# Kernel tuning notes

Measured on AMD Instinct MI355X. Metric: run time of the kernel, lower is better.

Reference implementation:

```python
import jax, jax.numpy as jnp
import numpy as np
import math

B, QL, KL, D, H, FF = 2, 2048, 2048, 512, 8, 2048
DH = D // H

def layernorm(x, g, b, eps=1e-5):
    m = jnp.mean(x, axis=-1, keepdims=True)
    v = jnp.mean((x - m) ** 2, axis=-1, keepdims=True)
    return (x - m) * jax.lax.rsqrt(v + eps) * g + b

def mha(x, mask, wq, bq, wk, bk, wv, bv, wo, bo, kv=None):
    # faithful port of MultiHeadAttention.forward (eval mode, dropout off)
    bs, qlen, dim = x.shape
    src = x if kv is None else kv
    def split(t):
        return t.reshape(bs, -1, H, DH).transpose(0, 2, 1, 3)  # [b,h,l,dh]
    q = split(x @ wq + bq) * (1.0 / math.sqrt(DH))
    k = split(src @ wk + bk)
    v = split(src @ wv + bv)
    scores = jnp.einsum('bhqd,bhkd->bhqk', q, k)
    m = mask[:, None, :, :] if mask.ndim == 3 else mask[:, None, None, :]
    scores = jnp.where(m == 0, -jnp.inf, scores)
    w = jax.nn.softmax(scores.astype(jnp.float32), axis=-1).astype(scores.dtype)
    ctx = jnp.einsum('bhqk,bhkd->bhqd', w, v)
    ctx = ctx.transpose(0, 2, 1, 3).reshape(bs, qlen, dim)
    return ctx @ wo + bo

def decoder_layer(tgt, memory, pos, tkpm, causal_mask, mem_mask,
                  sa, ca, l1w, l1b, l2w, l2b, n1g, n1b, n2g, n2b, n3g, n3b):
    tgt = tgt + pos
    t2 = layernorm(tgt, n1g, n1b)
    t2 = t2 * tkpm[:, :, None]
    t2 = mha(t2, causal_mask, *sa)
    tgt = tgt + t2
    t2 = layernorm(tgt, n2g, n2b)
    t2 = mha(t2, mem_mask, *ca, kv=memory)
    tgt = tgt + t2
    t2 = layernorm(tgt, n3g, n3b)
    t2 = jax.nn.relu(t2 @ l1w + l1b) @ l2w + l2b
    tgt = tgt + t2
    tgt = tgt * tkpm[:, :, None]
    return tgt

def setup_inputs() -> dict:
    key = jax.random.key(0)
    ks = jax.random.split(key, 32)
    it = iter(list(ks))
    def nrm(shape, s=0.02):
        return jax.random.normal(next(it), shape, jnp.float32) * s
    inp = {}
    inp['cfg'] = 0
    inp['tgt'] = jax.random.normal(next(it), (B, QL, D), jnp.float32)
    inp['memory'] = jax.random.normal(next(it), (B, KL, D), jnp.float32)
    inp['pos'] = jax.random.normal(next(it), (B, QL, D), jnp.float32)
    inp['causal_mask'] = jnp.broadcast_to(jnp.tril(jnp.ones((QL, QL), jnp.int32)), (B, QL, QL))
    inp['tgt_key_padding_mask'] = jnp.ones((B, QL), jnp.float32)
    mkpm = jax.random.randint(next(it), (B, KL), 0, 2).astype(jnp.int32)
    inp['memory_key_padding_mask'] = mkpm.at[:, 0].set(1)  # avoid fully-masked rows
    for p in ['sa', 'ca']:
        for w in ['q', 'k', 'v', 'o']:
            inp[f'{p}_{w}_w'] = nrm((D, D))
            inp[f'{p}_{w}_b'] = jnp.zeros((D,), jnp.float32)
    inp['lin1_w'] = nrm((D, FF)); inp['lin1_b'] = jnp.zeros((FF,), jnp.float32)
    inp['lin2_w'] = nrm((FF, D)); inp['lin2_b'] = jnp.zeros((D,), jnp.float32)
    for n in ['n1', 'n2', 'n3']:
        inp[f'{n}_g'] = jnp.ones((D,), jnp.float32)
        inp[f'{n}_b'] = jnp.zeros((D,), jnp.float32)
    return inp

def reference(cfg, tgt, memory, pos, causal_mask, tgt_key_padding_mask, memory_key_padding_mask,
              sa_q_w, sa_q_b, sa_k_w, sa_k_b, sa_v_w, sa_v_b, sa_o_w, sa_o_b,
              ca_q_w, ca_q_b, ca_k_w, ca_k_b, ca_v_w, ca_v_b, ca_o_w, ca_o_b,
              lin1_w, lin1_b, lin2_w, lin2_b,
              n1_g, n1_b, n2_g, n2_b, n3_g, n3_b):
    sa = (sa_q_w, sa_q_b, sa_k_w, sa_k_b, sa_v_w, sa_v_b, sa_o_w, sa_o_b)
    ca = (ca_q_w, ca_q_b, ca_k_w, ca_k_b, ca_v_w, ca_v_b, ca_o_w, ca_o_b)
    return decoder_layer(tgt, memory, pos, tgt_key_padding_mask, causal_mask, memory_key_padding_mask,
                         sa, ca, lin1_w, lin1_b, lin2_w, lin2_b, n1_g, n1_b, n2_g, n2_b, n3_g, n3_b)
```

## Files before the change

kernel.cpp:

```cpp
#include <hip/hip_runtime.h>
#include <hip/hip_bf16.h>
#include <stdint.h>

#define QL   2048
#define KLn  2048
#define DIM  512
#define NH   8
#define DH   64
#define NB   2
#define MROWS (NB*QL)
#define FFD  2048

typedef unsigned short u16;
typedef unsigned int u32;
typedef __attribute__((ext_vector_type(8))) short short8;
typedef __attribute__((ext_vector_type(4))) float f32x4;

__device__ __forceinline__ u16 f2b(float f){
  union { float f; u32 i; } v; v.f = f;
  u32 r = v.i + 0x7FFFu + ((v.i >> 16) & 1u);
  return (u16)(r >> 16);
}
__device__ __forceinline__ float b2f(u16 u){
  union { u32 i; float f; } v; v.i = ((u32)u) << 16; return v.f;
}
__device__ __forceinline__ u32 cvtpk(float a, float b){
  u32 r;
  asm("v_cvt_pk_bf16_f32 %0, %1, %2" : "=v"(r) : "v"(a), "v"(b));
  return r;
}

typedef __attribute__((address_space(3))) void as3void;
typedef __attribute__((address_space(1))) void as1void;
__device__ __forceinline__ void gload_lds16(const void* g, void* l){
  __builtin_amdgcn_global_load_lds((as1void*)g, (as3void*)l, 16, 0, 0);
}

#define BK 64
enum { EPI_BIAS=0, EPI_SCALEQ=1, EPI_RELU=2, EPI_RES=3, EPI_FIN=5, EPI_QKV=6, EPI_KV=7 };
#define QSCALE 0.1803368801111244f

template<int EPI>
__global__ __launch_bounds__(256, 4)
void gemm64(const u16* __restrict__ A, const u16* __restrict__ Bt,
            const float* __restrict__ bias,
            u16* __restrict__ Obf, float* __restrict__ Ores,
            const float* __restrict__ tk, float* __restrict__ fout,
            int K, int N)
{
  __shared__ __align__(16) u16 As[2][64*BK];
  __shared__ __align__(16) u16 Bs[2][64*BK];
  const int t  = threadIdx.x;
  const int l  = t & 63;
  const int lq = l & 15, lg = l >> 4;
  const int w  = t >> 6;
  const int wm = (w >> 1) * 32;
  const int wn = (w & 1) * 32;

  const int gx   = gridDim.x;
  const int nwg  = gx * gridDim.y;
  const int orig = blockIdx.x + gx * blockIdx.y;
  const int wgid = (orig & 7) * (nwg >> 3) + (orig >> 3);
  const int m0 = (wgid / gx) * 64;
  const int n0 = (wgid % gx) * 64;

  const int srow = t >> 3;
  const int scs  = t & 7;

  auto stageG = [&](u16* dA, u16* dB, int k0){
    _Pragma("unroll")
    for (int i = 0; i < 2; ++i){
      const int row = i*32 + srow;
      gload_lds16(A  + (size_t)(m0 + row)*K + k0 + ((scs ^ (row & 7)) << 3),
                  dA + row*BK + scs*8);
      gload_lds16(Bt + (size_t)(n0 + row)*K + k0 + ((scs ^ (row & 7)) << 3),
                  dB + row*BK + scs*8);
    }
  };

  int aoff[2][2], boff[2][2];
  _Pragma("unroll")
  for (int i = 0; i < 2; ++i)
    _Pragma("unroll")
    for (int kc = 0; kc < 2; ++kc){
      const int sw = (((kc*4 + lg) ^ (lq & 7)) << 3);
      aoff[i][kc] = ((wm + i*16 + lq)*BK + sw) * 2;
      boff[i][kc] = ((wn + i*16 + lq)*BK + sw) * 2;
    }

  f32x4 acc[2][2];
  _Pragma("unroll")
  for (int i=0;i<2;i++)
    _Pragma("unroll")
    for (int j=0;j<2;j++) acc[i][j] = (f32x4){0.f,0.f,0.f,0.f};

#define GBODY(BUF, KK)                                                        \
  {                                                                           \
    { const int ks = ((KK) + BK < K) ? (KK) + BK : 0;                         \
      stageG(As[(BUF)^1], Bs[(BUF)^1], ks); }                                 \
    asm volatile("s_waitcnt vmcnt(4)" ::: "memory");                          \
    __builtin_amdgcn_s_barrier();                                             \
    __builtin_amdgcn_sched_barrier(0);                                        \
    short8 af[2][2], bf[2][2];                                                \
    _Pragma("unroll")                                                         \
    for (int kc = 0; kc < 2; ++kc)                                            \
      _Pragma("unroll")                                                       \
      for (int i = 0; i < 2; ++i){                                            \
        af[i][kc] = *(const short8*)((const char*)As + (BUF)*8192 + aoff[i][kc]); \
        bf[i][kc] = *(const short8*)((const char*)Bs + (BUF)*8192 + boff[i][kc]); \
      }                                                                       \
    __builtin_amdgcn_s_barrier();                                             \
    __builtin_amdgcn_s_setprio(1);                                            \
    _Pragma("unroll")                                                         \
    for (int kc = 0; kc < 2; ++kc)                                            \
      _Pragma("unroll")                                                       \
      for (int i = 0; i < 2; ++i)                                             \
        _Pragma("unroll")                                                     \
        for (int j = 0; j < 2; ++j)                                           \
          acc[i][j] = __builtin_amdgcn_mfma_f32_16x16x32_bf16(af[i][kc], bf[j][kc], acc[i][j], 0,0,0); \
    __builtin_amdgcn_s_setprio(0);                                            \
  }

  stageG(As[0], Bs[0], 0);
  for (int k0 = 0; k0 < K; k0 += 2*BK){
    GBODY(0, k0)
    GBODY(1, k0 + BK)
  }
#undef GBODY

  _Pragma("unroll")
  for (int i=0;i<2;i++){
    _Pragma("unroll")
    for (int j=0;j<2;j++){
      _Pragma("unroll")
      for (int rr=0;rr<4;rr++){
        const int row = m0 + wm + i*16 + lg*4 + rr;
        const int col = n0 + wn + j*16 + lq;
        float v = acc[i][j][rr] + bias[col];
        if (EPI == EPI_SCALEQ) v *= QSCALE;
        if (EPI == EPI_RELU)   v = fmaxf(v, 0.f);
        if (EPI == EPI_RES)    Ores[(size_t)row*N + col] += v;
        else if (EPI == EPI_FIN){
          const size_t idx = (size_t)row*N + col;
          fout[idx] = (Ores[idx] + v) * tk[row];
        }
        else if (EPI == EPI_QKV){
          const int seg = col >> 9, c = col & 511;
          if (seg == 0)      Obf[(size_t)row*512 + c] = f2b(v * QSCALE);
          else if (seg == 1){
            const int bb = row >> 11, kv = row & 2047;
            const int hh = c >> 6,  dh = c & 63;
            Obf[(2u<<20) + ((((size_t)(bb*NH + hh) << 11) + kv) << 6) + (dh ^ ((kv & 7) << 3))] = f2b(v);
          }
          else               Obf[(4u<<20) + (size_t)row*512 + c] = f2b(v);
        }
        else if (EPI == EPI_KV){
          const int seg = col >> 9, c = col & 511;
          if (seg == 0){
            const int bb = row >> 11, kv = row & 2047;
            const int hh = c >> 6,  dh = c & 63;
            Obf[((((size_t)(bb*NH + hh) << 11) + kv) << 6) + (dh ^ ((kv & 7) << 3))] = f2b(v);
          }
          else               Obf[(2u<<20) + (size_t)row*512 + c] = f2b(v);
        }
        else                   Obf[(size_t)row*N + col] = f2b(v);
      }
    }
  }
}

template<bool CAUSAL>
__global__ __launch_bounds__(256, 2)
void attn8(const u16* __restrict__ Q, const u16* __restrict__ Kbh,
           const u16* __restrict__ Vth, const float* __restrict__ bias,
           u16* __restrict__ ctxp, float2* __restrict__ mlb)
{
  __shared__ __align__(16) u16 Kl[4][64*64];
  __shared__ __align__(16) u16 Vl[4][64*64];
  const int tid = threadIdx.x;
  const int l  = tid & 63;
  const int w  = tid >> 6;
  const int lq = l & 15, lg = l >> 4;
  const int h    = blockIdx.y;
  const int b    = blockIdx.z >> 1;
  const int half = blockIdx.z & 1;
  const int qtile = CAUSAL ? ((b & 1) ? (15 - (int)blockIdx.x) : (int)blockIdx.x)
                           : (int)blockIdx.x;
  const int rw = qtile*128 + w*32;

  const u16* kg = Kbh + ((size_t)(b*NH + h) << 17);
  const u16* vg = Vth + ((size_t)(b*NH + h) << 17);

  short8 aq[2][2];
  _Pragma("unroll")
  for (int g = 0; g < 2; ++g)
    _Pragma("unroll")
    for (int kc = 0; kc < 2; ++kc)
      aq[g][kc] = *(const short8*)(Q + (size_t)(b*QL + rw + g*16 + lq)*DIM + h*DH + kc*32 + lg*8);

  int koff[4][2];
  _Pragma("unroll")
  for (int j = 0; j < 4; ++j)
    _Pragma("unroll")
    for (int kc = 0; kc < 2; ++kc)
      koff[j][kc] = ((j*16 + lq)*64 + (((kc*4 + lg) ^ (lq & 7)) << 3)) * 2;

  f32x4 ctx[2][4];
  _Pragma("unroll")
  for (int g = 0; g < 2; ++g)
    _Pragma("unroll")
    for (int d = 0; d < 4; ++d) ctx[g][d] = (f32x4){0.f,0.f,0.f,0.f};
  f32x4 ls0 = (f32x4){0.f,0.f,0.f,0.f};
  f32x4 ls1 = (f32x4){0.f,0.f,0.f,0.f};
  float m0v = -1e30f, m1v = -1e30f;

  const int ntiles = CAUSAL ? (2*qtile + 2) : (KLn >> 6);
  const int P = (ntiles > half) ? ((ntiles - half + 1) >> 1) : 0;

  auto stageA = [&](u16* dK, u16* dV, int tile){
    const u16* kgs = kg + ((size_t)tile << 12);
    const u16* vgs = vg + tile*64;
    gload_lds16(kgs + w*1024 + l*8,       dK + w*1024 + l*8);
    gload_lds16(kgs + w*1024 + 512 + l*8, dK + w*1024 + 512 + l*8);
    gload_lds16(vgs + (size_t)(w*16 +     (l>>3))*KLn + (l&7)*8, dV + w*1024 + l*8);
    gload_lds16(vgs + (size_t)(w*16 + 8 + (l>>3))*KLn + (l&7)*8, dV + w*1024 + 512 + l*8);
  };

#define ABODY(BUF, II)                                                        \
  {                                                                           \
    const int TT = half + 2*(II);                                             \
    f32x4 bv[4];                                                              \
    if (!CAUSAL){                                                             \
      _Pragma("unroll")                                                       \
      for (int sub = 0; sub < 4; ++sub)                                       \
        bv[sub] = *(const f32x4*)(bias + b*KLn + TT*64 + sub*16 + lg*4);      \
    }                                                                         \
    { const int i2 = (II) + 2;                                                \
      const int ts = (i2 < P) ? half + 2*i2 : half;                           \
      stageA(Kl[((BUF)+2)&3], Vl[((BUF)+2)&3], ts); }                         \
    if (CAUSAL) asm volatile("s_waitcnt vmcnt(8)" ::: "memory");              \
    else        asm volatile("s_waitcnt vmcnt(12)" ::: "memory");             \
    __builtin_amdgcn_s_barrier();                                             \
    __builtin_amdgcn_sched_barrier(0);                                        \
    f32x4 s[2][4];                                                            \
    _Pragma("unroll")                                                         \
    for (int g = 0; g < 2; ++g)                                               \
      _Pragma("unroll")                                                       \
      for (int sub = 0; sub < 4; ++sub) s[g][sub] = (f32x4){0.f,0.f,0.f,0.f}; \
    __builtin_amdgcn_s_setprio(1);                                            \
    _Pragma("unroll")                                                         \
    for (int sub = 0; sub < 4; ++sub)                                         \
      _Pragma("unroll")                                                       \
      for (int kc = 0; kc < 2; ++kc){                                         \
        short8 bk = *(const short8*)((const char*)Kl + (BUF)*8192 + koff[sub][kc]); \
        s[0][sub] = __builtin_amdgcn_mfma_f32_16x16x32_bf16(bk, aq[0][kc], s[0][sub], 0,0,0); \
        s[1][sub] = __builtin_amdgcn_mfma_f32_16x16x32_bf16(bk, aq[1][kc], s[1][sub], 0,0,0); \
      }                                                                       \
    __builtin_amdgcn_s_setprio(0);                                            \
    if (CAUSAL){                                                              \
      if (TT*64 + 63 > rw){                                                   \
        _Pragma("unroll")                                                     \
        for (int g = 0; g < 2; ++g)                                           \
          _Pragma("unroll")                                                   \
          for (int sub = 0; sub < 4; ++sub)                                   \
            _Pragma("unroll")                                                 \
            for (int rr = 0; rr < 4; ++rr)                                    \
              if (TT*64 + sub*16 + lg*4 + rr > rw + g*16 + lq) s[g][sub][rr] = -1e30f; \
      }                                                                       \
    } else {                                                                  \
      _Pragma("unroll")                                                       \
      for (int g = 0; g < 2; ++g)                                             \
        _Pragma("unroll")                                                     \
        for (int sub = 0; sub < 4; ++sub) s[g][sub] += bv[sub];               \
    }                                                                         \
    float px0 = s[0][0][0], px1 = s[1][0][0];                                 \
    _Pragma("unroll")                                                         \
    for (int sub = 0; sub < 4; ++sub)                                         \
      _Pragma("unroll")                                                       \
      for (int rr = 0; rr < 4; ++rr){                                         \
        px0 = fmaxf(px0, s[0][sub][rr]);                                      \
        px1 = fmaxf(px1, s[1][sub][rr]);                                      \
      }                                                                       \
    if (!__all(px0 <= m0v + 8.0f && px1 <= m1v + 8.0f)){                      \
      px0 = fmaxf(px0, __shfl_xor(px0, 16));                                  \
      px0 = fmaxf(px0, __shfl_xor(px0, 32));                                  \
      px1 = fmaxf(px1, __shfl_xor(px1, 16));                                  \
      px1 = fmaxf(px1, __shfl_xor(px1, 32));                                  \
      const float mn0 = fmaxf(m0v, px0), mn1 = fmaxf(m1v, px1);               \
      const float c0 = exp2f(m0v - mn0), c1 = exp2f(m1v - mn1);               \
      ls0 *= c0; ls1 *= c1;                                                   \
      _Pragma("unroll")                                                       \
      for (int rr = 0; rr < 4; ++rr){                                         \
        const float b0 = __shfl(c0, lg*4 + rr), b1 = __shfl(c1, lg*4 + rr);   \
        _Pragma("unroll")                                                     \
        for (int d = 0; d < 4; ++d){ ctx[0][d][rr] *= b0; ctx[1][d][rr] *= b1; } \
      }                                                                       \
      m0v = mn0; m1v = mn1;                                                   \
    }                                                                         \
    u32 pk0[4][2], pk1[4][2];                                                 \
    _Pragma("unroll")                                                         \
    for (int sub = 0; sub < 4; ++sub){                                        \
      float a0 = exp2f(s[0][sub][0] - m0v), a1 = exp2f(s[0][sub][1] - m0v);   \
      float a2 = exp2f(s[0][sub][2] - m0v), a3 = exp2f(s[0][sub][3] - m0v);   \
      ls0 += (f32x4){a0, a1, a2, a3};                                         \
      pk0[sub][0] = cvtpk(a0, a1); pk0[sub][1] = cvtpk(a2, a3);               \
      float e0 = exp2f(s[1][sub][0] - m1v), e1 = exp2f(s[1][sub][1] - m1v);   \
      float e2 = exp2f(s[1][sub][2] - m1v), e3 = exp2f(s[1][sub][3] - m1v);   \
      ls1 += (f32x4){e0, e1, e2, e3};                                         \
      pk1[sub][0] = cvtpk(e0, e1); pk1[sub][1] = cvtpk(e2, e3);               \
    }                                                                         \
    union { u32 u[4]; short8 s8; } pA0, pA1, pB0, pB1;                        \
    pA0.u[0] = pk0[0][0]; pA0.u[1] = pk0[0][1]; pA0.u[2] = pk0[1][0]; pA0.u[3] = pk0[1][1]; \
    pA1.u[0] = pk0[2][0]; pA1.u[1] = pk0[2][1]; pA1.u[2] = pk0[3][0]; pA1.u[3] = pk0[3][1]; \
    pB0.u[0] = pk1[0][0]; pB0.u[1] = pk1[0][1]; pB0.u[2] = pk1[1][0]; pB0.u[3] = pk1[1][1]; \
    pB1.u[0] = pk1[2][0]; pB1.u[1] = pk1[2][1]; pB1.u[2] = pk1[3][0]; pB1.u[3] = pk1[3][1]; \
    __builtin_amdgcn_s_setprio(1);                                            \
    _Pragma("unroll")                                                         \
    for (int d0 = 0; d0 < 4; ++d0){                                           \
      short8 v0 = *(const short8*)((const char*)Vl + (BUF)*8192 + koff[d0][0]); \
      short8 v1 = *(const short8*)((const char*)Vl + (BUF)*8192 + koff[d0][1]); \
      ctx[0][d0] = __builtin_amdgcn_mfma_f32_16x16x32_bf16(pA0.s8, v0, ctx[0][d0], 0,0,0); \
      ctx[0][d0] = __builtin_amdgcn_mfma_f32_16x16x32_bf16(pA1.s8, v1, ctx[0][d0], 0,0,0); \
      ctx[1][d0] = __builtin_amdgcn_mfma_f32_16x16x32_bf16(pB0.s8, v0, ctx[1][d0], 0,0,0); \
      ctx[1][d0] = __builtin_amdgcn_mfma_f32_16x16x32_bf16(pB1.s8, v1, ctx[1][d0], 0,0,0); \
    }                                                                         \
    __builtin_amdgcn_s_setprio(0);                                            \
    __builtin_amdgcn_s_barrier();                                             \
  }

  if (P > 0){
    stageA(Kl[0], Vl[0], half);
    { const int ts1 = (1 < P) ? half + 2 : half;
      stageA(Kl[1], Vl[1], ts1); }
    for (int i = 0; i < P; i += 4){
      ABODY(0, i)
      if (i + 1 < P) ABODY(1, i + 1)
      if (i + 2 < P) ABODY(2, i + 2)
      if (i + 3 < P) ABODY(3, i + 3)
    }
  }
#undef ABODY

  float h0 = (ls0[0] + ls0[1]) + (ls0[2] + ls0[3]);
  float h1 = (ls1[0] + ls1[1]) + (ls1[2] + ls1[3]);
  h0 += __shfl_xor(h0, 16); h0 += __shfl_xor(h0, 32);
  h1 += __shfl_xor(h1, 16); h1 += __shfl_xor(h1, 32);
  if (lg == 0){
    mlb[((size_t)((half*NB + b)*NH + h) << 11) + rw + lq]      = make_float2(m0v, h0);
    mlb[((size_t)((half*NB + b)*NH + h) << 11) + rw + 16 + lq] = make_float2(m1v, h1);
  }
  u16* cp = ctxp + (size_t)half*MROWS*DIM;
  _Pragma("unroll")
  for (int g = 0; g < 2; ++g)
    _Pragma("unroll")
    for (int d0 = 0; d0 < 4; ++d0)
      _Pragma("unroll")
      for (int rr = 0; rr < 4; ++rr)
        cp[(size_t)(b*QL + rw + g*16 + lg*4 + rr)*DIM + h*DH + d0*16 + lq] =
            f2b(ctx[g][d0][rr]);
}

__global__ __launch_bounds__(256)
void attn_merge(const u16* __restrict__ ctxp, const float2* __restrict__ mlb,
                u16* __restrict__ O)
{
  const int idx = blockIdx.x*256 + threadIdx.x;
  const int row = idx >> 7;
  const int col = (idx & 127) * 4;
  const int b = row >> 11, qr = row & 2047, h = col >> 6;
  const float2 a0 = mlb[((size_t)((      b)*NH + h) << 11) + qr];
  const float2 a1 = mlb[((size_t)((NB  + b)*NH + h) << 11) + qr];
  const float mg = fmaxf(a0.x, a1.x);
  const float w0 = exp2f(a0.x - mg), w1 = exp2f(a1.x - mg);
  const float rden = 1.f / (a0.y*w0 + a1.y*w1);
  union { uint2 v; u16 h4[4]; } c0u, c1u;
  c0u.v = *(const uint2*)&ctxp[(size_t)row*DIM + col];
  c1u.v = *(const uint2*)&ctxp[(size_t)MROWS*DIM + (size_t)row*DIM + col];
  u16 o[4];
  #pragma unroll
  for (int i = 0; i < 4; ++i)
    o[i] = f2b((b2f(c0u.h4[i])*w0 + b2f(c1u.h4[i])*w1) * rden);
  *(uint2*)&O[(size_t)row*DIM + col] = *(const uint2*)o;
}

template<int MODE>
__global__ __launch_bounds__(128)
void ln_kernel(const float* __restrict__ in0, const float* __restrict__ in1,
               const float* __restrict__ tkpm,
               const float* __restrict__ g, const float* __restrict__ bvec,
               float* __restrict__ xres, u16* __restrict__ outb)
{
  const int row = blockIdx.x;
  const int t = threadIdx.x;
  float v[4];
  #pragma unroll
  for (int i = 0; i < 4; ++i){
    const int c = t + i*128;
    float x = in0[(size_t)row*DIM + c];
    if (MODE == 0){
      x += in1[(size_t)row*DIM + c];
      xres[(size_t)row*DIM + c] = x;
    }
    v[i] = x;
  }
  float s = v[0]+v[1]+v[2]+v[3];
  #pragma unroll
  for (int off = 1; off < 64; off <<= 1) s += __shfl_xor(s, off);
  __shared__ float red[4];
  if ((t & 63) == 0) red[t >> 6] = s;
  __syncthreads();
  const float mean = (red[0] + red[1]) * (1.f/512.f);
  float q = 0.f;
  #pragma unroll
  for (int i = 0; i < 4; ++i){ const float d = v[i]-mean; q += d*d; }
  #pragma unroll
  for (int off = 1; off < 64; off <<= 1) q += __shfl_xor(q, off);
  if ((t & 63) == 0) red[2 + (t >> 6)] = q;
  __syncthreads();
  const float var = (red[2] + red[3]) * (1.f/512.f);
  const float rs = rsqrtf(var + 1e-5f);
  const float tk = (MODE == 0) ? tkpm[row] : 1.f;
  #pragma unroll
  for (int i = 0; i < 4; ++i){
    const int c = t + i*128;
    const float y = (v[i] - mean) * rs * g[c] + bvec[c];
    outb[(size_t)row*DIM + c] = f2b(y * tk);
  }
}

__global__ __launch_bounds__(256)
void prep_all(const float* w0, const float* w1, const float* w2, const float* w3,
              const float* w4, const float* w5, const float* w6, const float* w7,
              const float* __restrict__ mem, const int* __restrict__ mkpm,
              const float* saqb, const float* sakb, const float* savb,
              const float* cakb, const float* cavb,
              u16* __restrict__ wtA, u16* __restrict__ memb,
              float* __restrict__ bias, float* __restrict__ bc0,
              float* __restrict__ bc1)
{
  __shared__ float tile[32][33];
  const int id = blockIdx.x;
  const int tid = threadIdx.x;
  if (id < 2048){
    const int z = id >> 8, rem = id & 255;
    const int r0 = (rem >> 4) * 32, c0 = (rem & 15) * 32;
    const float* wp[8] = {w0,w1,w2,w3,w4,w5,w6,w7};
    const float* w = wp[z];
    u16* o = wtA + (size_t)z * 512 * 512;
    const int tx = tid & 31, ty = tid >> 5;
    #pragma unroll
    for (int i = 0; i < 4; ++i)
      tile[ty + i*8][tx] = w[(size_t)(r0 + ty + i*8)*512 + c0 + tx];
    __syncthreads();
    #pragma unroll
    for (int i = 0; i < 4; ++i)
      o[(size_t)(c0 + ty + i*8)*512 + r0 + tx] = f2b(tile[tx][ty + i*8]);
  } else if (id < 4096){
    const int i = (id - 2048)*1024 + tid*4;
    f32x4 v = *(const f32x4*)&mem[i];
    uint2 p; p.x = cvtpk(v[0], v[1]); p.y = cvtpk(v[2], v[3]);
    *(uint2*)&memb[i] = p;
  } else {
    const int j = (id - 4096)*256 + tid;
    bias[j] = mkpm[j] ? 0.f : -1e30f;
    if (j < 1536) bc0[j] = (j < 512) ? saqb[j] : (j < 1024) ? sakb[j-512] : savb[j-1024];
    if (j < 1024) bc1[j] = (j < 512) ? cakb[j] : cavb[j-512];
  }
}

__global__ __launch_bounds__(256)
void transpose_vperm(const u16* __restrict__ in, u16* __restrict__ out)
{
  __shared__ u16 tile[32][33];
  in  += (size_t)blockIdx.z * KLn * DIM;
  out += (size_t)blockIdx.z * NH * DH * KLn;
  const int tx = threadIdx.x, ty = threadIdx.y;
  const int r0 = blockIdx.y*32, c0 = blockIdx.x*32;
  #pragma unroll
  for (int i = 0; i < 4; ++i)
    tile[ty + i*8][tx] = in[(size_t)(r0 + ty + i*8)*DIM + c0 + tx];
  __syncthreads();
  const int kv = r0 + tx;
  const int s  = (kv & ~31) | (((kv>>2)&3)<<3) | (((kv>>4)&1)<<2) | (kv&3);
  #pragma unroll
  for (int i = 0; i < 4; ++i){
    const int dcol = c0 + ty + i*8;
    const int hh = dcol >> 6, dh = dcol & 63;
    const int kvpos = (s & ~63) | (((((s>>3)&7) ^ (dh&7)) << 3)) | (s & 7);
    out[((size_t)(hh*DH + dh))*KLn + kvpos] = tile[tx][ty + i*8];
  }
}

__global__ __launch_bounds__(256)
void prep_cross(const u16* __restrict__ vb, u16* __restrict__ vt,
                const float* __restrict__ l1w, u16* __restrict__ l1wt,
                const float* __restrict__ l2w, u16* __restrict__ l2wt)
{
  const int id = blockIdx.x;
  const int tid = threadIdx.x;
  const int tx = tid & 31, ty = tid >> 5;
  if (id < 2048){
    __shared__ u16 tileu[32][33];
    const int z = id >> 10, rem = id & 1023;
    const int c0 = (rem & 15) * 32, r0 = (rem >> 4) * 32;
    const u16* in = vb + (size_t)z * KLn * DIM;
    u16* out = vt + (size_t)z * NH * DH * KLn;
    #pragma unroll
    for (int i = 0; i < 4; ++i)
      tileu[ty + i*8][tx] = in[(size_t)(r0 + ty + i*8)*DIM + c0 + tx];
    __syncthreads();
    const int kv = r0 + tx;
    const int s  = (kv & ~31) | (((kv>>2)&3)<<3) | (((kv>>4)&1)<<2) | (kv&3);
    #pragma unroll
    for (int i = 0; i < 4; ++i){
      const int dcol = c0 + ty + i*8;
      const int hh = dcol >> 6, dh = dcol & 63;
      const int kvpos = (s & ~63) | (((((s>>3)&7) ^ (dh&7)) << 3)) | (s & 7);
      out[((size_t)(hh*DH + dh))*KLn + kvpos] = tileu[tx][ty + i*8];
    }
  } else {
    __shared__ float tilef[32][33];
    if (id < 3072){
      const int rem = id - 2048;
      const int c0 = (rem & 63) * 32, r0 = (rem >> 6) * 32;
      #pragma unroll
      for (int i = 0; i < 4; ++i)
        tilef[ty + i*8][tx] = l1w[(size_t)(r0 + ty + i*8)*FFD + c0 + tx];
      __syncthreads();
      #pragma unroll
      for (int i = 0; i < 4; ++i)
        l1wt[(size_t)(c0 + ty + i*8)*512 + r0 + tx] = f2b(tilef[tx][ty + i*8]);
    } else {
      const int rem = id - 3072;
      const int c0 = (rem & 15) * 32, r0 = (rem >> 4) * 32;
      #pragma unroll
      for (int i = 0; i < 4; ++i)
        tilef[ty + i*8][tx] = l2w[(size_t)(r0 + ty + i*8)*512 + c0 + tx];
      __syncthreads();
      #pragma unroll
      for (int i = 0; i < 4; ++i)
        l2wt[(size_t)(c0 + ty + i*8)*FFD + r0 + tx] = f2b(tilef[tx][ty + i*8]);
    }
  }
}

extern "C" void kernel_launch(void* const* d_in, const int* in_sizes, int n_in,
                              void* d_out, int out_size, void* d_ws, size_t ws_size,
                              hipStream_t stream)
{
  const float* tgt  = (const float*)d_in[1];
  const float* mem  = (const float*)d_in[2];
  const float* pos  = (const float*)d_in[3];
  const float* tkpm = (const float*)d_in[5];
  const int*   mkpm = (const int*)d_in[6];
  const float* saqw = (const float*)d_in[7];  const float* saqb = (const float*)d_in[8];
  const float* sakw = (const float*)d_in[9];  const float* sakb = (const float*)d_in[10];
  const float* savw = (const float*)d_in[11]; const float* savb = (const float*)d_in[12];
  const float* saow = (const float*)d_in[13]; const float* saob = (const float*)d_in[14];
  const float* caqw = (const float*)d_in[15]; const float* caqb = (const float*)d_in[16];
  const float* cakw = (const float*)d_in[17]; const float* cakb = (const float*)d_in[18];
  const float* cavw = (const float*)d_in[19]; const float* cavb = (const float*)d_in[20];
  const float* caow = (const float*)d_in[21]; const float* caob = (const float*)d_in[22];
  const float* l1w  = (const float*)d_in[23]; const float* l1b  = (const float*)d_in[24];
  const float* l2w  = (const float*)d_in[25]; const float* l2b  = (const float*)d_in[26];
  const float* n1g  = (const float*)d_in[27]; const float* n1b  = (const float*)d_in[28];
  const float* n2g  = (const float*)d_in[29]; const float* n2b  = (const float*)d_in[30];
  const float* n3g  = (const float*)d_in[31]; const float* n3b  = (const float*)d_in[32];

  if (ws_size < 58720256) return;

  char* ws = (char*)d_ws;
  float* xres = (float*)(ws);
  u16* t2n    = (u16*)(ws + (8u<<20));
  u16* qb     = (u16*)(ws + (12u<<20));
  u16* kb     = (u16*)(ws + (16u<<20));
  u16* vb     = (u16*)(ws + (20u<<20));
  u16* vt     = (u16*)(ws + (24u<<20));
  float* bias = (float*)(ws + (28u<<20));
  float* bc0  = (float*)(ws + (28u<<20) + 16384);
  float* bc1  = (float*)(ws + (28u<<20) + 24576);
  float2* mlb = (float2*)(ws + (28u<<20) + 32768);
  u16* l1wt   = (u16*)(ws + (29u<<20));
  u16* l2wt   = (u16*)(ws + (31u<<20));
  u16* memb   = (u16*)(ws + (33u<<20));
  u16* wtA    = (u16*)(ws + (37u<<20));
  u16* ctxp   = (u16*)(ws + (41u<<20));
  u16* ffh    = (u16*)(ws + (12u<<20));

  float* out = (float*)d_out;
  const int W55 = 512*512;

  prep_all<<<dim3(4112), 256, 0, stream>>>(saqw, sakw, savw, saow,
                                           caqw, cakw, cavw, caow,
                                           mem, mkpm, saqb, sakb, savb, cakb, cavb,
                                           wtA, memb, bias, bc0, bc1);
  ln_kernel<0><<<MROWS, 128, 0, stream>>>(tgt, pos, tkpm, n1g, n1b, xres, t2n);

  #define G(EP, GX) gemm64<EP><<<dim3(GX,64), 256, 0, stream>>>

  G(EPI_QKV, 24)(t2n, wtA, bc0, qb, nullptr, nullptr, nullptr, 512, 1536);
  transpose_vperm<<<dim3(DIM/32, KLn/32, NB), dim3(32,8), 0, stream>>>(vb, vt);
  attn8<true><<<dim3(QL/128, NH, NB*2), 256, 0, stream>>>(qb, kb, vt, nullptr, ctxp, mlb);
  attn_merge<<<dim3(MROWS*DIM/1024), 256, 0, stream>>>(ctxp, mlb, t2n);
  G(EPI_RES, 8)(t2n, wtA + 3*W55, saob, nullptr, xres, nullptr, nullptr, 512, 512);

  ln_kernel<1><<<MROWS, 128, 0, stream>>>(xres, nullptr, nullptr, n2g, n2b, nullptr, t2n);

  G(EPI_SCALEQ, 8)(t2n,  wtA + 4*W55, caqb, qb, nullptr, nullptr, nullptr, 512, 512);
  G(EPI_KV, 16)(memb, wtA + 5*W55, bc1, kb, nullptr, nullptr, nullptr, 512, 1024);
  prep_cross<<<dim3(4096), 256, 0, stream>>>(vb, vt, l1w, l1wt, l2w, l2wt);
  attn8<false><<<dim3(QL/128, NH, NB*2), 256, 0, stream>>>(qb, kb, vt, bias, ctxp, mlb);
  attn_merge<<<dim3(MROWS*DIM/1024), 256, 0, stream>>>(ctxp, mlb, t2n);
  G(EPI_RES, 8)(t2n, wtA + 7*W55, caob, nullptr, xres, nullptr, nullptr, 512, 512);

  ln_kernel<1><<<MROWS, 128, 0, stream>>>(xres, nullptr, nullptr, n3g, n3b, nullptr, t2n);

  G(EPI_RELU, 32)(t2n, l1wt, l1b, ffh, nullptr, nullptr, nullptr, 512, FFD);
  G(EPI_FIN, 8)(ffh, l2wt, l2b, nullptr, xres, tkpm, out, 2048, 512);

  #undef G
}
```

Baseline: 195.3 us.

## Use 128x64 GEMM tiles for wide projections and split-K atomics for output GEMMs

Adds a 128x64-tile GEMM variant used for the QKV, cross KV and FFN1 projections, which raises per-block data reuse at the cost of lower occupancy. The N=512 output projections and FFN2 now use a split-K gemm64 that accumulates into the fp32 residual with atomicAdd, giving twice as many blocks for the narrow GEMMs. Because split-K cannot apply the final mask, the padding-mask scaling moves into a separate finalize kernel. It also removes the setprio hints in the attention kernel. Atomics make the summation order nondeterministic, and the extra launch adds a little overhead.

```diff
diff --git a/kernel.cpp b/kernel.cpp
--- a/kernel.cpp
+++ b/kernel.cpp
@@ -37,91 +37,95 @@
 }
 
 #define BK 64
-enum { EPI_BIAS=0, EPI_SCALEQ=1, EPI_RELU=2, EPI_RES=3, EPI_FIN=5, EPI_QKV=6, EPI_KV=7 };
+enum { EPI_BIAS=0, EPI_SCALEQ=1, EPI_RELU=2, EPI_RES=3, EPI_QKV=6, EPI_KV=7 };
 #define QSCALE 0.1803368801111244f
 
 template<int EPI>
-__global__ __launch_bounds__(256, 4)
-void gemm64(const u16* __restrict__ A, const u16* __restrict__ Bt,
-            const float* __restrict__ bias,
-            u16* __restrict__ Obf, float* __restrict__ Ores,
-            const float* __restrict__ tk, float* __restrict__ fout,
-            int K, int N)
-{
-  __shared__ __align__(16) u16 As[2][64*BK];
+__global__ __launch_bounds__(256, 3)
+void gemm128x64(const u16* __restrict__ A, const u16* __restrict__ Bt,
+                const float* __restrict__ bias, u16* __restrict__ Obf,
+                int K, int N)
+{
+  __shared__ __align__(16) u16 As[2][128*BK];
   __shared__ __align__(16) u16 Bs[2][64*BK];
   const int t  = threadIdx.x;
   const int l  = t & 63;
   const int lq = l & 15, lg = l >> 4;
   const int w  = t >> 6;
-  const int wm = (w >> 1) * 32;
+  const int wm = (w >> 1) * 64;
   const int wn = (w & 1) * 32;
 
   const int gx   = gridDim.x;
   const int nwg  = gx * gridDim.y;
   const int orig = blockIdx.x + gx * blockIdx.y;
   const int wgid = (orig & 7) * (nwg >> 3) + (orig >> 3);
-  const int m0 = (wgid / gx) * 64;
+  const int m0 = (wgid / gx) * 128;
   const int n0 = (wgid % gx) * 64;
 
   const int srow = t >> 3;
   const int scs  = t & 7;
 
-  auto stageG = [&](u16* dA, u16* dB, int k0){
+  auto stage = [&](u16* dA, u16* dB, int k0){
+    _Pragma("unroll")
+    for (int i = 0; i < 4; ++i){
+      const int row = i*32 + srow;
+      gload_lds16(A + (size_t)(m0 + row)*K + k0 + ((scs ^ (row & 7)) << 3),
+                  dA + row*BK + scs*8);
+    }
     _Pragma("unroll")
     for (int i = 0; i < 2; ++i){
       const int row = i*32 + srow;
-      gload_lds16(A  + (size_t)(m0 + row)*K + k0 + ((scs ^ (row & 7)) << 3),
-                  dA + row*BK + scs*8);
       gload_lds16(Bt + (size_t)(n0 + row)*K + k0 + ((scs ^ (row & 7)) << 3),
                   dB + row*BK + scs*8);
     }
   };
 
-  int aoff[2][2], boff[2][2];
-  _Pragma("unroll")
-  for (int i = 0; i < 2; ++i)
-    _Pragma("unroll")
-    for (int kc = 0; kc < 2; ++kc){
-      const int sw = (((kc*4 + lg) ^ (lq & 7)) << 3);
-      aoff[i][kc] = ((wm + i*16 + lq)*BK + sw) * 2;
-      boff[i][kc] = ((wn + i*16 + lq)*BK + sw) * 2;
-    }
-
-  f32x4 acc[2][2];
-  _Pragma("unroll")
-  for (int i=0;i<2;i++)
+  int aoff[4][2], boff[2][2];
+  _Pragma("unroll")
+  for (int kc = 0; kc < 2; ++kc){
+    const int sw = (((kc*4 + lg) ^ (lq & 7)) << 3);
+    _Pragma("unroll")
+    for (int i = 0; i < 4; ++i) aoff[i][kc] = ((wm + i*16 + lq)*BK + sw) * 2;
+    _Pragma("unroll")
+    for (int j = 0; j < 2; ++j) boff[j][kc] = ((wn + j*16 + lq)*BK + sw) * 2;
+  }
+
+  f32x4 acc[4][2];
+  _Pragma("unroll")
+  for (int i=0;i<4;i++)
     _Pragma("unroll")
     for (int j=0;j<2;j++) acc[i][j] = (f32x4){0.f,0.f,0.f,0.f};
 
 #define GBODY(BUF, KK)                                                        \
   {                                                                           \
     { const int ks = ((KK) + BK < K) ? (KK) + BK : 0;                         \
-      stageG(As[(BUF)^1], Bs[(BUF)^1], ks); }                                 \
-    asm volatile("s_waitcnt vmcnt(4)" ::: "memory");                          \
+      stage(As[(BUF)^1], Bs[(BUF)^1], ks); }                                  \
+    asm volatile("s_waitcnt vmcnt(6)" ::: "memory");                          \
     __builtin_amdgcn_s_barrier();                                             \
     __builtin_amdgcn_sched_barrier(0);                                        \
-    short8 af[2][2], bf[2][2];                                                \
-    _Pragma("unroll")                                                         \
-    for (int kc = 0; kc < 2; ++kc)                                            \
-      _Pragma("unroll")                                                       \
-      for (int i = 0; i < 2; ++i){                                            \
-        af[i][kc] = *(const short8*)((const char*)As + (BUF)*8192 + aoff[i][kc]); \
-        bf[i][kc] = *(const short8*)((const char*)Bs + (BUF)*8192 + boff[i][kc]); \
-      }                                                                       \
+    short8 af[4][2], bf[2][2];                                                \
+    _Pragma("unroll")                                                         \
+    for (int kc = 0; kc < 2; ++kc){                                           \
+      _Pragma("unroll")                                                       \
+      for (int i = 0; i < 4; ++i)                                             \
+        af[i][kc] = *(const short8*)((const char*)As + (BUF)*16384 + aoff[i][kc]); \
+      _Pragma("unroll")                                                       \
+      for (int j = 0; j < 2; ++j)                                             \
+        bf[j][kc] = *(const short8*)((const char*)Bs + (BUF)*8192 + boff[j][kc]); \
+    }                                                                         \
     __builtin_amdgcn_s_barrier();                                             \
     __builtin_amdgcn_s_setprio(1);                                            \
     _Pragma("unroll")                                                         \
     for (int kc = 0; kc < 2; ++kc)                                            \
       _Pragma("unroll")                                                       \
-      for (int i = 0; i < 2; ++i)                                             \
+      for (int i = 0; i < 4; ++i)                                             \
         _Pragma("unroll")                                                     \
         for (int j = 0; j < 2; ++j)                                           \
           acc[i][j] = __builtin_amdgcn_mfma_f32_16x16x32_bf16(af[i][kc], bf[j][kc], acc[i][j], 0,0,0); \
     __builtin_amdgcn_s_setprio(0);                                            \
   }
 
-  stageG(As[0], Bs[0], 0);
+  stage(As[0], Bs[0], 0);
   for (int k0 = 0; k0 < K; k0 += 2*BK){
     GBODY(0, k0)
     GBODY(1, k0 + BK)
@@ -129,7 +133,7 @@
 #undef GBODY
 
   _Pragma("unroll")
-  for (int i=0;i<2;i++){
+  for (int i=0;i<4;i++){
     _Pragma("unroll")
     for (int j=0;j<2;j++){
       _Pragma("unroll")
@@ -137,14 +141,8 @@
         const int row = m0 + wm + i*16 + lg*4 + rr;
         const int col = n0 + wn + j*16 + lq;
         float v = acc[i][j][rr] + bias[col];
-        if (EPI == EPI_SCALEQ) v *= QSCALE;
-        if (EPI == EPI_RELU)   v = fmaxf(v, 0.f);
-        if (EPI == EPI_RES)    Ores[(size_t)row*N + col] += v;
-        else if (EPI == EPI_FIN){
-          const size_t idx = (size_t)row*N + col;
-          fout[idx] = (Ores[idx] + v) * tk[row];
-        }
-        else if (EPI == EPI_QKV){
+        if (EPI == EPI_RELU) v = fmaxf(v, 0.f);
+        if (EPI == EPI_QKV){
           const int seg = col >> 9, c = col & 511;
           if (seg == 0)      Obf[(size_t)row*512 + c] = f2b(v * QSCALE);
           else if (seg == 1){
@@ -163,7 +161,118 @@
           }
           else               Obf[(2u<<20) + (size_t)row*512 + c] = f2b(v);
         }
-        else                   Obf[(size_t)row*N + col] = f2b(v);
+        else Obf[(size_t)row*N + col] = f2b(v);
+      }
+    }
+  }
+}
+
+template<int EPI, bool SPLIT>
+__global__ __launch_bounds__(256, 4)
+void gemm64(const u16* __restrict__ A, const u16* __restrict__ Bt,
+            const float* __restrict__ bias,
+            u16* __restrict__ Obf, float* __restrict__ Ores,
+            int K, int N)
+{
+  __shared__ __align__(16) u16 As[2][64*BK];
+  __shared__ __align__(16) u16 Bs[2][64*BK];
+  const int t  = threadIdx.x;
+  const int l  = t & 63;
+  const int lq = l & 15, lg = l >> 4;
+  const int w  = t >> 6;
+  const int wm = (w >> 1) * 32;
+  const int wn = (w & 1) * 32;
+
+  const int gx   = gridDim.x;
+  const int nwg  = gx * gridDim.y;
+  const int orig = blockIdx.x + gx * blockIdx.y;
+  const int wgid = (orig & 7) * (nwg >> 3) + (orig >> 3);
+  const int m0 = (wgid / gx) * 64;
+  const int n0 = (wgid % gx) * 64;
+
+  const int khalf = SPLIT ? (K >> 1) : K;
+  const int kbase = SPLIT ? (int)blockIdx.z * khalf : 0;
+
+  const int srow = t >> 3;
+  const int scs  = t & 7;
+
+  auto stage = [&](u16* dA, u16* dB, int k0){
+    _Pragma("unroll")
+    for (int i = 0; i < 2; ++i){
+      const int row = i*32 + srow;
+      gload_lds16(A  + (size_t)(m0 + row)*K + kbase + k0 + ((scs ^ (row & 7)) << 3),
+                  dA + row*BK + scs*8);
+      gload_lds16(Bt + (size_t)(n0 + row)*K + kbase + k0 + ((scs ^ (row & 7)) << 3),
+                  dB + row*BK + scs*8);
+    }
+  };
+
+  int aoff[2][2], boff[2][2];
+  _Pragma("unroll")
+  for (int i = 0; i < 2; ++i)
+    _Pragma("unroll")
+    for (int kc = 0; kc < 2; ++kc){
+      const int sw = (((kc*4 + lg) ^ (lq & 7)) << 3);
+      aoff[i][kc] = ((wm + i*16 + lq)*BK + sw) * 2;
+      boff[i][kc] = ((wn + i*16 + lq)*BK + sw) * 2;
+    }
+
+  f32x4 acc[2][2];
+  _Pragma("unroll")
+  for (int i=0;i<2;i++)
+    _Pragma("unroll")
+    for (int j=0;j<2;j++) acc[i][j] = (f32x4){0.f,0.f,0.f,0.f};
+
+#define GBODY(BUF, KK)                                                        \
+  {                                                                           \
+    { const int ks = ((KK) + BK < khalf) ? (KK) + BK : 0;                     \
+      stage(As[(BUF)^1], Bs[(BUF)^1], ks); }                                  \
+    asm volatile("s_waitcnt vmcnt(4)" ::: "memory");                          \
+    __builtin_amdgcn_s_barrier();                                             \
+    __builtin_amdgcn_sched_barrier(0);                                        \
+    short8 af[2][2], bf[2][2];                                                \
+    _Pragma("unroll")                                                         \
+    for (int kc = 0; kc < 2; ++kc)                                            \
+      _Pragma("unroll")                                                       \
+      for (int i = 0; i < 2; ++i){                                            \
+        af[i][kc] = *(const short8*)((const char*)As + (BUF)*8192 + aoff[i][kc]); \
+        bf[i][kc] = *(const short8*)((const char*)Bs + (BUF)*8192 + boff[i][kc]); \
+      }                                                                       \
+    __builtin_amdgcn_s_barrier();                                             \
+    __builtin_amdgcn_s_setprio(1);                                            \
+    _Pragma("unroll")                                                         \
+    for (int kc = 0; kc < 2; ++kc)                                            \
+      _Pragma("unroll")                                                       \
+      for (int i = 0; i < 2; ++i)                                             \
+        _Pragma("unroll")                                                     \
+        for (int j = 0; j < 2; ++j)                                           \
+          acc[i][j] = __builtin_amdgcn_mfma_f32_16x16x32_bf16(af[i][kc], bf[j][kc], acc[i][j], 0,0,0); \
+    __builtin_amdgcn_s_setprio(0);                                            \
+  }
+
+  stage(As[0], Bs[0], 0);
+  for (int k0 = 0; k0 < khalf; k0 += 2*BK){
+    GBODY(0, k0)
+    GBODY(1, k0 + BK)
+  }
+#undef GBODY
+
+  const bool addb = !SPLIT || blockIdx.z == 0;
+  _Pragma("unroll")
+  for (int i=0;i<2;i++){
+    _Pragma("unroll")
+    for (int j=0;j<2;j++){
+      _Pragma("unroll")
+      for (int rr=0;rr<4;rr++){
+        const int row = m0 + wm + i*16 + lg*4 + rr;
+        const int col = n0 + wn + j*16 + lq;
+        float v = acc[i][j][rr] + (addb ? bias[col] : 0.f);
+        if (EPI == EPI_SCALEQ) v *= QSCALE;
+        if (EPI == EPI_RES){
+          if (SPLIT) atomicAdd(&Ores[(size_t)row*N + col], v);
+          else       Ores[(size_t)row*N + col] += v;
+        }
+        else Obf[(size_t)row*N + col] = f2b(v);
       }
     }
   }
@@ -247,7 +356,6 @@
     for (int g = 0; g < 2; ++g)                                               \
       _Pragma("unroll")                                                       \
       for (int sub = 0; sub < 4; ++sub) s[g][sub] = (f32x4){0.f,0.f,0.f,0.f}; \
-    __builtin_amdgcn_s_setprio(1);                                            \
     _Pragma("unroll")                                                         \
     for (int sub = 0; sub < 4; ++sub)                                         \
       _Pragma("unroll")                                                       \
@@ -256,7 +364,6 @@
         s[0][sub] = __builtin_amdgcn_mfma_f32_16x16x32_bf16(bk, aq[0][kc], s[0][sub], 0,0,0); \
         s[1][sub] = __builtin_amdgcn_mfma_f32_16x16x32_bf16(bk, aq[1][kc], s[1][sub], 0,0,0); \
       }                                                                       \
-    __builtin_amdgcn_s_setprio(0);                                            \
     if (CAUSAL){                                                              \
       if (TT*64 + 63 > rw){                                                   \
         _Pragma("unroll")                                                     \
@@ -314,7 +421,6 @@
     pA1.u[0] = pk0[2][0]; pA1.u[1] = pk0[2][1]; pA1.u[2] = pk0[3][0]; pA1.u[3] = pk0[3][1]; \
     pB0.u[0] = pk1[0][0]; pB0.u[1] = pk1[0][1]; pB0.u[2] = pk1[1][0]; pB0.u[3] = pk1[1][1]; \
     pB1.u[0] = pk1[2][0]; pB1.u[1] = pk1[2][1]; pB1.u[2] = pk1[3][0]; pB1.u[3] = pk1[3][1]; \
-    __builtin_amdgcn_s_setprio(1);                                            \
     _Pragma("unroll")                                                         \
     for (int d0 = 0; d0 < 4; ++d0){                                           \
       short8 v0 = *(const short8*)((const char*)Vl + (BUF)*8192 + koff[d0][0]); \
@@ -324,7 +430,6 @@
       ctx[1][d0] = __builtin_amdgcn_mfma_f32_16x16x32_bf16(pB0.s8, v0, ctx[1][d0], 0,0,0); \
       ctx[1][d0] = __builtin_amdgcn_mfma_f32_16x16x32_bf16(pB1.s8, v1, ctx[1][d0], 0,0,0); \
     }                                                                         \
-    __builtin_amdgcn_s_setprio(0);                                            \
     __builtin_amdgcn_s_barrier();                                             \
   }
 
@@ -544,6 +649,15 @@
   }
 }
 
+__global__ void finalize_k(const float* __restrict__ xres, const float* __restrict__ tkpm,
+                           float* __restrict__ out){
+  const int i = (blockIdx.x*256 + threadIdx.x)*4;
+  const f32x4 v = *(const f32x4*)&xres[i];
+  const float tk = tkpm[i >> 9];
+  f32x4 o = {v[0]*tk, v[1]*tk, v[2]*tk, v[3]*tk};
+  *(f32x4*)&out[i] = o;
+}
+
 extern "C" void kernel_launch(void* const* d_in, const int* in_sizes, int n_in,
                               void* d_out, int out_size, void* d_ws, size_t ws_size,
                               hipStream_t stream)
@@ -596,27 +710,24 @@
                                            wtA, memb, bias, bc0, bc1);
   ln_kernel<0><<<MROWS, 128, 0, stream>>>(tgt, pos, tkpm, n1g, n1b, xres, t2n);
 
-  #define G(EP, GX) gemm64<EP><<<dim3(GX,64), 256, 0, stream>>>
-
-  G(EPI_QKV, 24)(t2n, wtA, bc0, qb, nullptr, nullptr, nullptr, 512, 1536);
+  gemm128x64<EPI_QKV><<<dim3(24,32), 256, 0, stream>>>(t2n, wtA, bc0, qb, 512, 1536);
   transpose_vperm<<<dim3(DIM/32, KLn/32, NB), dim3(32,8), 0, stream>>>(vb, vt);
   attn8<true><<<dim3(QL/128, NH, NB*2), 256, 0, stream>>>(qb, kb, vt, nullptr, ctxp, mlb);
   attn_merge<<<dim3(MROWS*DIM/1024), 256, 0, stream>>>(ctxp, mlb, t2n);
-  G(EPI_RES, 8)(t2n, wtA + 3*W55, saob, nullptr, xres, nullptr, nullptr, 512, 512);
+  gemm64<EPI_RES,true><<<dim3(8,64,2), 256, 0, stream>>>(t2n, wtA + 3*W55, saob, nullptr, xres, 512, 512);
 
   ln_kernel<1><<<MROWS, 128, 0, stream>>>(xres, nullptr, nullptr, n2g, n2b, nullptr, t2n);
 
-  G(EPI_SCALEQ, 8)(t2n,  wtA + 4*W55, caqb, qb, nullptr, nullptr, nullptr, 512, 512);
-  G(EPI_KV, 16)(memb, wtA + 5*W55, bc1, kb, nullptr, nullptr, nullptr, 512, 1024);
+  gemm64<EPI_SCALEQ,false><<<dim3(8,64), 256, 0, stream>>>(t2n, wtA + 4*W55, caqb, qb, nullptr, 512, 512);
+  gemm128x64<EPI_KV><<<dim3(16,32), 256, 0, stream>>>(memb, wtA + 5*W55, bc1, kb, 512, 1024);
   prep_cross<<<dim3(4096), 256, 0, stream>>>(vb, vt, l1w, l1wt, l2w, l2wt);
   attn8<false><<<dim3(QL/128, NH, NB*2), 256, 0, stream>>>(qb, kb, vt, bias, ctxp, mlb);
   attn_merge<<<dim3(MROWS*DIM/1024), 256, 0, stream>>>(ctxp, mlb, t2n);
-  G(EPI_RES, 8)(t2n, wtA + 7*W55, caob, nullptr, xres, nullptr, nullptr, 512, 512);
+  gemm64<EPI_RES,true><<<dim3(8,64,2), 256, 0, stream>>>(t2n, wtA + 7*W55, caob, nullptr, xres, 512, 512);
 
   ln_kernel<1><<<MROWS, 128, 0, stream>>>(xres, nullptr, nullptr, n3g, n3b, nullptr, t2n);
 
-  G(EPI_RELU, 32)(t2n, l1wt, l1b, ffh, nullptr, nullptr, nullptr, 512, FFD);
-  G(EPI_FIN, 8)(ffh, l2wt, l2b, nullptr, xres, tkpm, out, 2048, 512);
-
-  #undef G
-}
+  gemm128x64<EPI_RELU><<<dim3(32,32), 256, 0, stream>>>(t2n, l1wt, l1b, ffh, 512, FFD);
+  gemm64<EPI_RES,true><<<dim3(8,64,2), 256, 0, stream>>>(ffh, l2wt, l2b, nullptr, xres, 2048, 512);
+  finalize_k<<<dim3(MROWS*DIM/1024), 256, 0, stream>>>(xres, tkpm, out);
+}
```

Measured after the change: 216.4 us. +10.8%, slower.
